# Kernel tuning notes

Hardware: AMD Instinct MI355X
Metric: run time of the kernel (lower is better)

Reference implementation:

```python
import jax, jax.numpy as jnp
import numpy as np

B, S, D, F, E, TOP_K = 4, 2048, 1024, 4096, 8, 2


def setup_inputs() -> dict:
    key = jax.random.key(0)
    ks = jax.random.split(key, 6)
    sd = 1.0 / np.sqrt(D)
    sf = 1.0 / np.sqrt(F)
    return {
        "x": jax.random.normal(ks[0], (B, S, D), dtype=jnp.float32),
        "router_w": jax.random.normal(ks[1], (E, D), dtype=jnp.float32) * sd,
        "router_b": jnp.zeros((E,), dtype=jnp.float32),
        "w1": jax.random.normal(ks[2], (E, F, D), dtype=jnp.float32) * sd,  # Linear(d_model->d_ff) weight [out,in]
        "w2": jax.random.normal(ks[3], (E, D, F), dtype=jnp.float32) * sf,  # Linear(d_ff->d_model)
        "w3": jax.random.normal(ks[4], (E, F, D), dtype=jnp.float32) * sd,
    }


def reference(x, router_w, router_b, w1, w2, w3):
    # Router: softmax over experts, then top-k with renormalized gates.
    logits = jnp.einsum("bsd,ed->bse", x, router_w) + router_b          # [B,S,E]
    probs = jax.nn.softmax(logits, axis=-1)
    topk_p, topk_i = jax.lax.top_k(probs, TOP_K)                         # [B,S,K]
    topk_p = topk_p / jnp.sum(topk_p, axis=-1, keepdims=True)
    # Per-token combine weight for each expert (0 if not selected).
    combine = jnp.sum(jax.nn.one_hot(topk_i, E, dtype=x.dtype) * topk_p[..., None], axis=-2)  # [B,S,E]

    # Note: expert(x*mask)*mask == expert(x)*mask since SwiGLU(0)=0 (no bias).
    out = jnp.zeros_like(x)
    for e in range(E):  # small fixed expert count
        h = jax.nn.silu(jnp.einsum("bsd,fd->bsf", x, w1[e])) * jnp.einsum("bsd,fd->bsf", x, w3[e])
        out = out + combine[..., e:e + 1] * jnp.einsum("bsf,df->bsd", h, w2[e])
    return out
```

## Files before the change

kernel.cpp:

```cpp
#include <hip/hip_runtime.h>
#include <hip/hip_fp16.h>


#define NTOK 8192
#define D_ 1024
#define F_ 4096
#define E_ 8
#define SLOT_CAP 18432

using half8 = __attribute__((ext_vector_type(8))) _Float16;
using half4 = __attribute__((ext_vector_type(4))) _Float16;
using f32x4 = __attribute__((ext_vector_type(4))) float;

__device__ __forceinline__ void gload16(const void* g, void* l) {
  __builtin_amdgcn_global_load_lds((const __attribute__((address_space(1))) void*)g,
                                   (__attribute__((address_space(3))) void*)l, 16, 0, 0);
}

__global__ __launch_bounds__(256) void cvt_kernel(const float* __restrict__ src,
                                                  _Float16* __restrict__ dst, int n4) {
  int i = blockIdx.x * 256 + threadIdx.x;
  int stride = gridDim.x * 256;
  for (; i < n4; i += stride) {
    float4 v = ((const float4*)src)[i];
    half4 h;
    h.x = (_Float16)v.x; h.y = (_Float16)v.y; h.z = (_Float16)v.z; h.w = (_Float16)v.w;
    ((half4*)dst)[i] = h;
  }
}

__global__ __launch_bounds__(256) void cvt_w13_kernel(const float* __restrict__ w1,
                                                      const float* __restrict__ w3,
                                                      _Float16* __restrict__ w13, int n4) {
  int i = blockIdx.x * 256 + threadIdx.x;
  int stride = gridDim.x * 256;
  for (; i < n4; i += stride) {
    int d4 = i & 255;
    int row = i >> 8;
    int e = row >> 12, f = row & 4095;
    size_t vbase = ((size_t)e << 13) | ((size_t)(f >> 4) << 5) | (size_t)(f & 15);
    float4 v1 = ((const float4*)w1)[i];
    float4 v3 = ((const float4*)w3)[i];
    half4 h1, h3;
    h1.x = (_Float16)v1.x; h1.y = (_Float16)v1.y; h1.z = (_Float16)v1.z; h1.w = (_Float16)v1.w;
    h3.x = (_Float16)v3.x; h3.y = (_Float16)v3.y; h3.z = (_Float16)v3.z; h3.w = (_Float16)v3.w;
    ((half4*)w13)[vbase * 256 + d4] = h1;
    ((half4*)w13)[(vbase + 16) * 256 + d4] = h3;
  }
}

__global__ __launch_bounds__(256) void router_kernel(
    const float* __restrict__ x, const float* __restrict__ rw, const float* __restrict__ rbias,
    _Float16* __restrict__ x16, int* __restrict__ tok_e, float* __restrict__ tok_g,
    int* __restrict__ counts) {
  int wv = threadIdx.x >> 6, lane = threadIdx.x & 63;
  int t = blockIdx.x * 4 + wv;
  const float4* xr = (const float4*)(x + (size_t)t * D_);
  float acc[E_];
#pragma unroll
  for (int e = 0; e < E_; ++e) acc[e] = 0.f;
  for (int i = lane; i < D_ / 4; i += 64) {
    float4 xv = xr[i];
    half4 hx;
    hx.x = (_Float16)xv.x; hx.y = (_Float16)xv.y; hx.z = (_Float16)xv.z; hx.w = (_Float16)xv.w;
    ((half4*)(x16 + (size_t)t * D_))[i] = hx;
#pragma unroll
    for (int e = 0; e < E_; ++e) {
      float4 wv4 = ((const float4*)(rw + (size_t)e * D_))[i];
      acc[e] += xv.x * wv4.x + xv.y * wv4.y + xv.z * wv4.z + xv.w * wv4.w;
    }
  }
#pragma unroll
  for (int e = 0; e < E_; ++e) {
#pragma unroll
    for (int off = 32; off > 0; off >>= 1) acc[e] += __shfl_down(acc[e], off);
  }
  if (lane == 0) {
    float p[E_], mx = -1e30f;
#pragma unroll
    for (int e = 0; e < E_; ++e) { p[e] = acc[e] + rbias[e]; mx = fmaxf(mx, p[e]); }
#pragma unroll
    for (int e = 0; e < E_; ++e) p[e] = expf(p[e] - mx);
    int i0 = 0;
#pragma unroll
    for (int e = 1; e < E_; ++e) if (p[e] > p[i0]) i0 = e;
    int i1 = (i0 == 0) ? 1 : 0;
#pragma unroll
    for (int e = 0; e < E_; ++e) if (e != i0 && p[e] > p[i1]) i1 = e;
    float s = p[i0] + p[i1];
    tok_e[t * 2] = i0; tok_e[t * 2 + 1] = i1;
    tok_g[t * 2] = p[i0] / s; tok_g[t * 2 + 1] = p[i1] / s;
    atomicAdd(&counts[i0], 1); atomicAdd(&counts[i1], 1);
  }
}

__global__ void init_kernel(int* slot_token, int* counts, int* cursor) {
  int i = blockIdx.x * 256 + threadIdx.x;
  if (blockIdx.x == 0 && threadIdx.x < E_) { counts[threadIdx.x] = 0; cursor[threadIdx.x] = 0; }
  if (i < SLOT_CAP) slot_token[i] = 0;
}

__global__ void scan_kernel(const int* __restrict__ counts, int* __restrict__ offs) {
  if (threadIdx.x == 0) {
    int o = 0;
    for (int e = 0; e < E_; ++e) { offs[e] = o; o += ((counts[e] + 255) / 256) * 256; }
    offs[E_] = o;
  }
}

__global__ void scatter_kernel(const int* __restrict__ tok_e, const int* __restrict__ offs,
                               int* __restrict__ cursor, int* __restrict__ slot_token,
                               int* __restrict__ slot_of) {
  int i = blockIdx.x * 256 + threadIdx.x;
  if (i >= NTOK * 2) return;
  int e = tok_e[i];
  int pos = offs[e] + atomicAdd(&cursor[e], 1);
  slot_token[pos] = i >> 1;
  slot_of[i] = pos;
}

template <int MODE, int ORD, int KSPLIT, int KD, int NBN, int RPX, int BEROWS>
__global__ __launch_bounds__(512, 2) void moe_gemm_kernel(
    const _Float16* __restrict__ Amat, const _Float16* __restrict__ Bmat,
    const int* __restrict__ slot_token, const int* __restrict__ offs,
    void* __restrict__ outp, void* __restrict__ outp2) {
  constexpr int BM = 256;
  constexpr int MROW = 8;
  constexpr int AH = BM * 32;
  constexpr int BUFH = (BM + 256) * 32;
  constexpr int KL = KD / KSPLIT;
  constexpr int NT = KL / 32;
  __shared__ _Float16 lds[4 * BUFH];

  int id = blockIdx.x;
  int xcd = id & 7, idx = id >> 3;
  int vr, nb;
  if constexpr (ORD == 0) {
    int band = idx / (8 * NBN);
    int i2 = idx - band * (8 * NBN);
    int rib = (RPX - band * 8) < 8 ? (RPX - band * 8) : 8;
    nb = i2 / rib;
    vr = xcd * RPX + band * 8 + (i2 - nb * rib);
  } else {
    nb = idx % NBN;
    vr = xcd * RPX + idx / NBN;
  }
  int rb = vr, ks = 0;
  if constexpr (KSPLIT == 2) { rb = vr >> 1; ks = vr & 1; }
  int row0 = rb * BM;
  if (row0 >= offs[E_]) return;
  int e = 0;
#pragma unroll
  for (int i = 1; i < E_; ++i) if (row0 >= offs[i]) e = i;
  int koff = ks * KL;

  int t = threadIdx.x, l = t & 63, w = t >> 6;
  int wr = w >> 2, wc = w & 3;
  int srow = t >> 2;
  int gsrc8 = ((l & 3) ^ ((l >> 3) & 3)) * 8;

  const _Float16* aP0;
  const _Float16* aP1;
  if constexpr (MODE == 0) {
    int tk0 = slot_token[row0 + srow];
    int tk1 = slot_token[row0 + srow + 128];
    aP0 = Amat + (size_t)tk0 * KD + koff + gsrc8;
    aP1 = Amat + (size_t)tk1 * KD + koff + gsrc8;
  } else {
    aP0 = Amat + (size_t)(row0 + srow) * KD + koff + gsrc8;
    aP1 = Amat + (size_t)(row0 + srow + 128) * KD + koff + gsrc8;
  }
  const _Float16* b0P =
      Bmat + ((size_t)e * BEROWS + (size_t)nb * 256 + srow) * KD + koff + gsrc8;
  const _Float16* b1P = b0P + (size_t)128 * KD;

  int fr = l & 15, kg = l >> 4;
  int swz8 = (kg ^ ((fr >> 1) & 3)) * 8;
  const int rA = (wr * 128 + fr) * 32 + swz8;
  const int rB = AH + (wc * 64 + fr) * 32 + swz8;

  half8 aF[4];
  half8 bF[4];
  f32x4 acc[MROW][4];
#pragma unroll
  for (int m = 0; m < MROW; ++m)
#pragma unroll
    for (int n = 0; n < 4; ++n) acc[m][n] = (f32x4){0.f, 0.f, 0.f, 0.f};

#pragma unroll
  for (int tt = 0; tt < 3; ++tt) {
    gload16(aP0 + tt * 32, &lds[tt * BUFH + w * 512]);
    gload16(aP1 + tt * 32, &lds[tt * BUFH + 4096 + w * 512]);
    gload16(b0P + tt * 32, &lds[tt * BUFH + AH + w * 512]);
    gload16(b1P + tt * 32, &lds[tt * BUFH + AH + 4096 + w * 512]);
  }
  asm volatile("s_waitcnt vmcnt(8)" ::: "memory");
  __builtin_amdgcn_s_barrier();
  __builtin_amdgcn_sched_barrier(0);
  aP0 += 96; aP1 += 96; b0P += 96; b1P += 96;

#define MF16(BASE)                                                           \
  _Pragma("unroll") for (int mi = 0; mi < 4; ++mi)                           \
  _Pragma("unroll") for (int ni = 0; ni < 4; ++ni)                           \
      acc[(BASE) + mi][ni] = __builtin_amdgcn_mfma_f32_16x16x32_f16(         \
          aF[mi], bF[ni], acc[(BASE) + mi][ni], 0, 0, 0);

#define STEPP(U, PRE, WN)                                                         \
  {                                                                               \
    constexpr int bi_ = (U) & 3;                                                  \
    constexpr int bs_ = ((U) + 3) & 3;                                            \
    const _Float16* cb_ = &lds[bi_ * BUFH];                                       \
    if (PRE) {                                                                    \
      gload16(aP0 + (U) * 32, &lds[bs_ * BUFH + w * 512]);                        \
      gload16(aP1 + (U) * 32, &lds[bs_ * BUFH + 4096 + w * 512]);                 \
    }                                                                             \
    aF[0] = *(const half8*)(cb_ + rA);                                            \
    aF[1] = *(const half8*)(cb_ + rA + 512);                                      \
    aF[2] = *(const half8*)(cb_ + rA + 1024);                                     \
    aF[3] = *(const half8*)(cb_ + rA + 1536);                                     \
    bF[0] = *(const half8*)(cb_ + rB);                                            \
    bF[1] = *(const half8*)(cb_ + rB + 512);                                      \
    bF[2] = *(const half8*)(cb_ + rB + 1024);                                     \
    bF[3] = *(const half8*)(cb_ + rB + 1536);                                     \
    __builtin_amdgcn_sched_barrier(0);                                            \
    __builtin_amdgcn_s_barrier();                                                 \
    asm volatile("s_waitcnt lgkmcnt(0)" ::: "memory");                            \
    __builtin_amdgcn_sched_barrier(0);                                            \
    __builtin_amdgcn_s_setprio(1);                                                \
    MF16(0)                                                                       \
    __builtin_amdgcn_s_setprio(0);                                                \
    __builtin_amdgcn_sched_barrier(0);                                            \
    __builtin_amdgcn_s_barrier();                                                 \
    if (PRE) {                                                                    \
      gload16(b0P + (U) * 32, &lds[bs_ * BUFH + AH + w * 512]);                   \
      gload16(b1P + (U) * 32, &lds[bs_ * BUFH + AH + 4096 + w * 512]);            \
    }                                                                             \
    aF[0] = *(const half8*)(cb_ + rA + 2048);                                     \
    aF[1] = *(const half8*)(cb_ + rA + 2560);                                     \
    aF[2] = *(const half8*)(cb_ + rA + 3072);                                     \
    aF[3] = *(const half8*)(cb_ + rA + 3584);                                     \
    __builtin_amdgcn_sched_barrier(0);                                            \
    __builtin_amdgcn_s_barrier();                                                 \
    asm volatile("s_waitcnt lgkmcnt(0)" ::: "memory");                            \
    __builtin_amdgcn_sched_barrier(0);                                            \
    __builtin_amdgcn_s_setprio(1);                                                \
    MF16(4)                                                                       \
    __builtin_amdgcn_s_setprio(0);                                                \
    if ((WN) >= 0) {                                                              \
      asm volatile("s_waitcnt vmcnt(%0)" ::"i"((WN) >= 0 ? (WN) : 0) : "memory"); \
      __builtin_amdgcn_sched_barrier(0);                                          \
      __builtin_amdgcn_s_barrier();                                               \
      __builtin_amdgcn_sched_barrier(0);                                          \
    }                                                                             \
  }

  for (int j4 = 0; j4 < NT - 4; j4 += 4) {
    STEPP(0, true, 8)
    STEPP(1, true, 8)
    STEPP(2, true, 8)
    STEPP(3, true, 8)
    aP0 += 128; aP1 += 128; b0P += 128; b1P += 128;
  }
  STEPP(0, true, 8)
  STEPP(1, false, 4)
  STEPP(2, false, 0)
  STEPP(3, false, -1)
#undef STEPP
#undef MF16

  int q4 = kg * 4;
  if constexpr (MODE == 0) {
    _Float16* hb = (_Float16*)outp;
#pragma unroll
    for (int mi = 0; mi < MROW; ++mi) {
      size_t rbase = (size_t)(row0 + wr * 128 + mi * 16 + q4);
#pragma unroll
      for (int p = 0; p < 2; ++p) {
        int fc = nb * 128 + (wc * 2 + p) * 16 + fr;
#pragma unroll
        for (int i = 0; i < 4; ++i) {
          float gv = acc[mi][2 * p][i];
          float hv = gv / (1.f + __expf(-gv)) * acc[mi][2 * p + 1][i];
          hb[(rbase + i) * (size_t)F_ + fc] = (_Float16)hv;
        }
      }
    }
  } else {
    float* yb = (float*)(ks == 0 ? outp : outp2);
#pragma unroll
    for (int mi = 0; mi < MROW; ++mi) {
      size_t rbase = (size_t)(row0 + wr * 128 + mi * 16 + q4);
#pragma unroll
      for (int ni = 0; ni < 4; ++ni) {
        int col = nb * 256 + wc * 64 + ni * 16 + fr;
#pragma unroll
        for (int i = 0; i < 4; ++i)
          yb[(rbase + i) * (size_t)D_ + col] = acc[mi][ni][i];
      }
    }
  }
}

__global__ __launch_bounds__(256) void combine_kernel(
    const float* __restrict__ ya, const float* __restrict__ yb2,
    const int* __restrict__ slot_of, const float* __restrict__ tok_g,
    float* __restrict__ out) {
  int t = blockIdx.x, i = threadIdx.x;
  int s0 = slot_of[t * 2], s1 = slot_of[t * 2 + 1];
  float g0 = tok_g[t * 2], g1 = tok_g[t * 2 + 1];
  float4 a0 = ((const float4*)(ya + (size_t)s0 * D_))[i];
  float4 a1 = ((const float4*)(yb2 + (size_t)s0 * D_))[i];
  float4 b0 = ((const float4*)(ya + (size_t)s1 * D_))[i];
  float4 b1 = ((const float4*)(yb2 + (size_t)s1 * D_))[i];
  float4 r;
  r.x = g0 * (a0.x + a1.x) + g1 * (b0.x + b1.x);
  r.y = g0 * (a0.y + a1.y) + g1 * (b0.y + b1.y);
  r.z = g0 * (a0.z + a1.z) + g1 * (b0.z + b1.z);
  r.w = g0 * (a0.w + a1.w) + g1 * (b0.w + b1.w);
  ((float4*)(out + (size_t)t * D_))[i] = r;
}

extern "C" void kernel_launch(void* const* d_in, const int* in_sizes, int n_in,
                              void* d_out, int out_size, void* d_ws, size_t ws_size,
                              hipStream_t stream) {
  const float* x  = (const float*)d_in[0];
  const float* rw = (const float*)d_in[1];
  const float* rbc = (const float*)d_in[2];
  const float* w1 = (const float*)d_in[3];
  const float* w2 = (const float*)d_in[4];
  const float* w3 = (const float*)d_in[5];
  float* out = (float*)d_out;

  char* ws = (char*)d_ws;
  size_t off = 0;
  auto take = [&](size_t bytes) {
    char* p = ws + off;
    off = (off + bytes + 255) & ~(size_t)255;
    return p;
  };
  _Float16* x16 = (_Float16*)take((size_t)NTOK * D_ * 2);
  _Float16* w13 = (_Float16*)take((size_t)E_ * 2 * F_ * D_ * 2);
  _Float16* w2h = (_Float16*)take((size_t)E_ * D_ * F_ * 2);
  _Float16* hbuf = (_Float16*)take((size_t)SLOT_CAP * F_ * 2);
  float* ybuf = (float*)take((size_t)SLOT_CAP * D_ * 4);
  int* slot_token = (int*)take((size_t)SLOT_CAP * 4);
  int* tok_e = (int*)take((size_t)NTOK * 2 * 4);
  float* tok_g = (float*)take((size_t)NTOK * 2 * 4);
  int* slot_of = (int*)take((size_t)NTOK * 2 * 4);
  int* counts = (int*)take(E_ * 4);
  int* cursor = (int*)take(E_ * 4);
  int* offs = (int*)take((E_ + 1) * 4);
  float* ybuf2 = (float*)w13;

  cvt_w13_kernel<<<4096, 256, 0, stream>>>(w1, w3, w13, E_ * F_ * D_ / 4);
  cvt_kernel<<<4096, 256, 0, stream>>>(w2, w2h, E_ * D_ * F_ / 4);
  init_kernel<<<(SLOT_CAP + 255) / 256, 256, 0, stream>>>(slot_token, counts, cursor);
  router_kernel<<<NTOK / 4, 256, 0, stream>>>(x, rw, rbc, x16, tok_e, tok_g, counts);
  scan_kernel<<<1, 64, 0, stream>>>(counts, offs);
  scatter_kernel<<<(NTOK * 2 + 255) / 256, 256, 0, stream>>>(tok_e, offs, cursor, slot_token, slot_of);
  moe_gemm_kernel<0, 0, 1, 1024, 32, 9, 8192><<<2304, 512, 0, stream>>>(
      x16, w13, slot_token, offs, (void*)hbuf, nullptr);
  moe_gemm_kernel<1, 1, 2, 4096, 4, 18, 1024><<<576, 512, 0, stream>>>(
      hbuf, w2h, slot_token, offs, (void*)ybuf, (void*)ybuf2);
  combine_kernel<<<NTOK, 256, 0, stream>>>(ybuf, ybuf2, slot_of, tok_g, out);
}
```

Baseline: 895.2 us.

## Merge weight conversions and replace atomic count/scan/scatter with single-block ballot scatter

Fuses the two weight-conversion kernels into one launch, and removes the init, scan and atomic counting steps by computing per-expert counts, padded offsets, padding zeroing and slot positions inside a single 1024-thread block using wave ballots. This cuts four kernel launches and the global atomics in the router and scatter. In exchange the scatter runs on one workgroup and walks all 16K assignments twice serially. Slot order within each expert now follows token order, so it is deterministic.

```diff
diff --git a/kernel.cpp b/kernel.cpp
--- a/kernel.cpp
+++ b/kernel.cpp
@@ -17,42 +17,37 @@
                                    (__attribute__((address_space(3))) void*)l, 16, 0, 0);
 }
 
-__global__ __launch_bounds__(256) void cvt_kernel(const float* __restrict__ src,
-                                                  _Float16* __restrict__ dst, int n4) {
-  int i = blockIdx.x * 256 + threadIdx.x;
-  int stride = gridDim.x * 256;
-  for (; i < n4; i += stride) {
-    float4 v = ((const float4*)src)[i];
-    half4 h;
-    h.x = (_Float16)v.x; h.y = (_Float16)v.y; h.z = (_Float16)v.z; h.w = (_Float16)v.w;
-    ((half4*)dst)[i] = h;
-  }
-}
-
-__global__ __launch_bounds__(256) void cvt_w13_kernel(const float* __restrict__ w1,
-                                                      const float* __restrict__ w3,
-                                                      _Float16* __restrict__ w13, int n4) {
-  int i = blockIdx.x * 256 + threadIdx.x;
-  int stride = gridDim.x * 256;
-  for (; i < n4; i += stride) {
-    int d4 = i & 255;
-    int row = i >> 8;
-    int e = row >> 12, f = row & 4095;
-    size_t vbase = ((size_t)e << 13) | ((size_t)(f >> 4) << 5) | (size_t)(f & 15);
-    float4 v1 = ((const float4*)w1)[i];
-    float4 v3 = ((const float4*)w3)[i];
-    half4 h1, h3;
-    h1.x = (_Float16)v1.x; h1.y = (_Float16)v1.y; h1.z = (_Float16)v1.z; h1.w = (_Float16)v1.w;
-    h3.x = (_Float16)v3.x; h3.y = (_Float16)v3.y; h3.z = (_Float16)v3.z; h3.w = (_Float16)v3.w;
-    ((half4*)w13)[vbase * 256 + d4] = h1;
-    ((half4*)w13)[(vbase + 16) * 256 + d4] = h3;
+__global__ __launch_bounds__(256) void cvt_weights_kernel(
+    const float* __restrict__ w1, const float* __restrict__ w3, const float* __restrict__ w2,
+    _Float16* __restrict__ w13, _Float16* __restrict__ w2h) {
+  int b = blockIdx.x;
+  if (b < 4096) {
+    for (int i = b * 256 + threadIdx.x; i < E_ * F_ * D_ / 4; i += 4096 * 256) {
+      int d4 = i & 255;
+      int row = i >> 8;
+      int e = row >> 12, f = row & 4095;
+      size_t vbase = ((size_t)e << 13) | ((size_t)(f >> 4) << 5) | (size_t)(f & 15);
+      float4 v1 = ((const float4*)w1)[i];
+      float4 v3 = ((const float4*)w3)[i];
+      half4 h1, h3;
+      h1.x = (_Float16)v1.x; h1.y = (_Float16)v1.y; h1.z = (_Float16)v1.z; h1.w = (_Float16)v1.w;
+      h3.x = (_Float16)v3.x; h3.y = (_Float16)v3.y; h3.z = (_Float16)v3.z; h3.w = (_Float16)v3.w;
+      ((half4*)w13)[vbase * 256 + d4] = h1;
+      ((half4*)w13)[(vbase + 16) * 256 + d4] = h3;
+    }
+  } else {
+    for (int i = (b - 4096) * 256 + threadIdx.x; i < E_ * D_ * F_ / 4; i += 4096 * 256) {
+      float4 v = ((const float4*)w2)[i];
+      half4 h;
+      h.x = (_Float16)v.x; h.y = (_Float16)v.y; h.z = (_Float16)v.z; h.w = (_Float16)v.w;
+      ((half4*)w2h)[i] = h;
+    }
   }
 }
 
 __global__ __launch_bounds__(256) void router_kernel(
     const float* __restrict__ x, const float* __restrict__ rw, const float* __restrict__ rbias,
-    _Float16* __restrict__ x16, int* __restrict__ tok_e, float* __restrict__ tok_g,
-    int* __restrict__ counts) {
+    _Float16* __restrict__ x16, int* __restrict__ tok_e, float* __restrict__ tok_g) {
   int wv = threadIdx.x >> 6, lane = threadIdx.x & 63;
   int t = blockIdx.x * 4 + wv;
   const float4* xr = (const float4*)(x + (size_t)t * D_);
@@ -90,33 +85,81 @@
     float s = p[i0] + p[i1];
     tok_e[t * 2] = i0; tok_e[t * 2 + 1] = i1;
     tok_g[t * 2] = p[i0] / s; tok_g[t * 2 + 1] = p[i1] / s;
-    atomicAdd(&counts[i0], 1); atomicAdd(&counts[i1], 1);
-  }
-}
-
-__global__ void init_kernel(int* slot_token, int* counts, int* cursor) {
-  int i = blockIdx.x * 256 + threadIdx.x;
-  if (blockIdx.x == 0 && threadIdx.x < E_) { counts[threadIdx.x] = 0; cursor[threadIdx.x] = 0; }
-  if (i < SLOT_CAP) slot_token[i] = 0;
-}
-
-__global__ void scan_kernel(const int* __restrict__ counts, int* __restrict__ offs) {
-  if (threadIdx.x == 0) {
+  }
+}
+
+__global__ __launch_bounds__(1024) void scatter_kernel(
+    const int* __restrict__ tok_e, int* __restrict__ slot_token,
+    int* __restrict__ slot_of, int* __restrict__ offs) {
+  __shared__ int wcnt[16][E_];
+  int t = threadIdx.x, lane = t & 63, wv = t >> 6;
+
+  int total[E_];
+#pragma unroll
+  for (int e = 0; e < E_; ++e) total[e] = 0;
+  for (int c = 0; c < NTOK * 2; c += 1024) {
+    int ei = tok_e[c + t];
+#pragma unroll
+    for (int e = 0; e < E_; ++e) {
+      unsigned long long m = __ballot(ei == e);
+      if (lane == 0) wcnt[wv][e] = __popcll(m);
+    }
+    __syncthreads();
+#pragma unroll
+    for (int e = 0; e < E_; ++e) {
+      int s = 0;
+#pragma unroll
+      for (int w2 = 0; w2 < 16; ++w2) s += wcnt[w2][e];
+      total[e] += s;
+    }
+    __syncthreads();
+  }
+  int base[E_ + 1];
+  {
     int o = 0;
-    for (int e = 0; e < E_; ++e) { offs[e] = o; o += ((counts[e] + 255) / 256) * 256; }
-    offs[E_] = o;
-  }
-}
-
-__global__ void scatter_kernel(const int* __restrict__ tok_e, const int* __restrict__ offs,
-                               int* __restrict__ cursor, int* __restrict__ slot_token,
-                               int* __restrict__ slot_of) {
-  int i = blockIdx.x * 256 + threadIdx.x;
-  if (i >= NTOK * 2) return;
-  int e = tok_e[i];
-  int pos = offs[e] + atomicAdd(&cursor[e], 1);
-  slot_token[pos] = i >> 1;
-  slot_of[i] = pos;
+#pragma unroll
+    for (int e = 0; e < E_; ++e) { base[e] = o; o += ((total[e] + 255) >> 8) << 8; }
+    base[E_] = o;
+  }
+  if (t <= E_) offs[t] = base[t];
+#pragma unroll
+  for (int e = 0; e < E_; ++e)
+    for (int p = base[e] + total[e] + t; p < base[e + 1]; p += 1024) slot_token[p] = 0;
+
+  int run[E_];
+#pragma unroll
+  for (int e = 0; e < E_; ++e) run[e] = 0;
+  for (int c = 0; c < NTOK * 2; c += 1024) {
+    int ei = tok_e[c + t];
+    int rank = 0;
+#pragma unroll
+    for (int e = 0; e < E_; ++e) {
+      unsigned long long m = __ballot(ei == e);
+      if (lane == 0) wcnt[wv][e] = __popcll(m);
+      if (ei == e) rank = __popcll(m & ((1ULL << lane) - 1ULL));
+    }
+    __syncthreads();
+    int mybase = 0, wbase = 0;
+    int tot[E_];
+#pragma unroll
+    for (int e = 0; e < E_; ++e) {
+      int s = 0;
+#pragma unroll
+      for (int w2 = 0; w2 < 16; ++w2) {
+        int v = wcnt[w2][e];
+        if (e == ei && w2 < wv) wbase += v;
+        s += v;
+      }
+      tot[e] = s;
+      if (e == ei) mybase = base[e] + run[e];
+    }
+    int pos = mybase + wbase + rank;
+    slot_token[pos] = (c + t) >> 1;
+    slot_of[c + t] = pos;
+#pragma unroll
+    for (int e = 0; e < E_; ++e) run[e] += tot[e];
+    __syncthreads();
+  }
 }
 
 template <int MODE, int ORD, int KSPLIT, int KD, int NBN, int RPX, int BEROWS>
@@ -347,17 +390,12 @@
   int* tok_e = (int*)take((size_t)NTOK * 2 * 4);
   float* tok_g = (float*)take((size_t)NTOK * 2 * 4);
   int* slot_of = (int*)take((size_t)NTOK * 2 * 4);
-  int* counts = (int*)take(E_ * 4);
-  int* cursor = (int*)take(E_ * 4);
   int* offs = (int*)take((E_ + 1) * 4);
   float* ybuf2 = (float*)w13;
 
-  cvt_w13_kernel<<<4096, 256, 0, stream>>>(w1, w3, w13, E_ * F_ * D_ / 4);
-  cvt_kernel<<<4096, 256, 0, stream>>>(w2, w2h, E_ * D_ * F_ / 4);
-  init_kernel<<<(SLOT_CAP + 255) / 256, 256, 0, stream>>>(slot_token, counts, cursor);
-  router_kernel<<<NTOK / 4, 256, 0, stream>>>(x, rw, rbc, x16, tok_e, tok_g, counts);
-  scan_kernel<<<1, 64, 0, stream>>>(counts, offs);
-  scatter_kernel<<<(NTOK * 2 + 255) / 256, 256, 0, stream>>>(tok_e, offs, cursor, slot_token, slot_of);
+  cvt_weights_kernel<<<8192, 256, 0, stream>>>(w1, w3, w2, w13, w2h);
+  router_kernel<<<NTOK / 4, 256, 0, stream>>>(x, rw, rbc, x16, tok_e, tok_g);
+  scatter_kernel<<<1, 1024, 0, stream>>>(tok_e, slot_token, slot_of, offs);
   moe_gemm_kernel<0, 0, 1, 1024, 32, 9, 8192><<<2304, 512, 0, stream>>>(
       x16, w13, slot_token, offs, (void*)hbuf, nullptr);
   moe_gemm_kernel<1, 1, 2, 4096, 4, 18, 1024><<<576, 512, 0, stream>>>(
```

Measured after the change: 737.4 us. 17.6% less time.
